# Kernel tuning notes

Hardware: AMD Instinct MI355X
Metric: run time of the kernel (lower is better)

The kernel has to match this reference:

```python
import jax, jax.numpy as jnp
import numpy as np

B, G, D = 256, 64, 20          # batch, genes per term, subsystem output dim
T3, T2, T1, T0 = 2048, 512, 128, 1  # terms per stratum, deepest first
FAN = 4                        # children per internal term (root gets all T1)
EPS = 1e-5                     # BatchNorm1d eps


def setup_inputs() -> dict:
    key = jax.random.key(0)
    ks = jax.random.split(key, 32)
    def genes(k, T):
        # binary gene perturbation states (column 3 of go_gene_strata_state)
        return (jax.random.uniform(k, (B, T, G)) < 0.5).astype(jnp.float32)
    def lin(kw, kb, T, din):
        # nn.init.uniform_(w, -0.001, 0.001) per DCellSubsystem
        W = jax.random.uniform(kw, (T, din, D), minval=-0.001, maxval=0.001)
        b = jax.random.uniform(kb, (T, D), minval=-0.001, maxval=0.001)
        return W, b
    in3, in2, in1, in0 = G, FAN * D + G, FAN * D + G, T1 * D + G
    W3, b3 = lin(ks[0], ks[1], T3, in3)
    W2, b2 = lin(ks[2], ks[3], T2, in2)
    W1, b1 = lin(ks[4], ks[5], T1, in1)
    W0, b0 = lin(ks[6], ks[7], T0, in0)
    ones = lambda T: jnp.ones((T, D), jnp.float32)
    zeros = lambda T: jnp.zeros((T, D), jnp.float32)
    hw0 = jax.random.normal(ks[8], (T0, D, 1)) * 0.1
    hb0 = jnp.zeros((T0, 1), jnp.float32)
    return {
        'genes3': genes(ks[9], T3), 'genes2': genes(ks[10], T2),
        'genes1': genes(ks[11], T1), 'genes0': genes(ks[12], T0),
        'W3': W3, 'b3': b3, 'g3': ones(T3), 'be3': zeros(T3),
        'W2': W2, 'b2': b2, 'g2': ones(T2), 'be2': zeros(T2),
        'W1': W1, 'b1': b1, 'g1': ones(T1), 'be1': zeros(T1),
        'W0': W0, 'b0': b0, 'g0': ones(T0), 'be0': zeros(T0),
        'hw0': hw0, 'hb0': hb0,
    }


def _subsystem(x, W, b, g, be):
    # Linear -> BatchNorm1d (training mode, batch stats over axis 0) -> Tanh
    z = jnp.einsum('bti,tio->bto', x, W) + b          # [B, T, D]
    mu = jnp.mean(z, axis=0)
    var = jnp.var(z, axis=0)                           # biased, as in torch BN
    zn = (z - mu) * jax.lax.rsqrt(var + EPS)
    return jnp.tanh(zn * g + be)


def reference(genes3, genes2, genes1, genes0,
              W3, b3, g3, be3, W2, b2, g2, be2,
              W1, b1, g1, be1, W0, b0, g0, be0, hw0, hb0):
    # stratum 3 (leaves): input is gene states only
    h3 = _subsystem(genes3, W3, b3, g3, be3)           # [B, T3, D]
    # stratum 2: concat FAN contiguous children + own gene states
    x2 = jnp.concatenate([h3.reshape(B, T2, FAN * D), genes2], axis=-1)
    h2 = _subsystem(x2, W2, b2, g2, be2)               # [B, T2, D]
    x1 = jnp.concatenate([h2.reshape(B, T1, FAN * D), genes1], axis=-1)
    h1 = _subsystem(x1, W1, b1, g1, be1)               # [B, T1, D]
    # root: all T1 children + root gene states
    x0 = jnp.concatenate([h1.reshape(B, T0, T1 * D), genes0], axis=-1)
    h0 = _subsystem(x0, W0, b0, g0, be0)               # [B, 1, D]
    pred = jnp.einsum('bto,toc->btc', h0, hw0) + hb0   # root linear head
    return pred.reshape(B, 1)
```

## Files before the change

### kernel.cpp

```cpp
#include <hip/hip_runtime.h>
#include <hip/hip_fp16.h>


#define DEV static __device__ __forceinline__

constexpr int B_  = 256, G_ = 64, D_ = 20;
constexpr int T3_ = 2048, T2_ = 512, T1_ = 128;
constexpr float EPS_ = 1e-5f;

typedef unsigned char u8;

constexpr size_t OFF_GT3 = 0;
constexpr size_t SZ_GT3 = (size_t)T3_ * B_ * G_;
constexpr size_t OFF_GT2 = OFF_GT3 + SZ_GT3;
constexpr size_t SZ_GT2 = (size_t)T2_ * B_ * G_;
constexpr size_t OFF_GT1 = OFF_GT2 + SZ_GT2;
constexpr size_t SZ_GT1 = (size_t)T1_ * B_ * G_;
constexpr size_t OFF_H3B = OFF_GT1 + SZ_GT1;
constexpr size_t SZ_H3 = (size_t)T3_ * B_ * D_ * 2;
constexpr size_t OFF_H2B = OFF_H3B + SZ_H3;
constexpr size_t SZ_H2 = (size_t)T2_ * B_ * D_ * 2;
constexpr size_t OFF_H1B = OFF_H2B + SZ_H2;
constexpr size_t SZ_H1 = (size_t)B_ * T1_ * D_ * 4;
constexpr size_t OFF_Z0B = OFF_H1B + SZ_H1;

typedef _Float16 half8_t __attribute__((ext_vector_type(8)));
typedef float f32x4 __attribute__((ext_vector_type(4)));

DEV half8_t as_h8(uint4 u) {
    union { uint4 u4; half8_t h; } c; c.u4 = u; return c.h;
}

DEV half8_t u8x8_to_h8(uint2 v) {
    uint4 r;
    uint x = v.x;
    r.x = ((x & 0xFFu) | ((x & 0xFF00u) << 8)) * 0x3C00u;
    r.y = (((x >> 16) & 0xFFu) | ((x >> 8) & 0xFF0000u)) * 0x3C00u;
    x = v.y;
    r.z = ((x & 0xFFu) | ((x & 0xFF00u) << 8)) * 0x3C00u;
    r.w = (((x >> 16) & 0xFFu) | ((x >> 8) & 0xFF0000u)) * 0x3C00u;
    return as_h8(r);
}

DEV float fast_tanh(float x) {
    float e = __expf(2.0f * x);
    return fmaf(-2.0f, __builtin_amdgcn_rcpf(e + 1.0f), 1.0f);
}

constexpr int TRB = 8;
constexpr int TRT = 64;
constexpr int LROW = TRT * G_ / 4 + 4;

__global__ __launch_bounds__(256, 4) void k_transpose_all(
        const float* __restrict__ g3s, const float* __restrict__ g2s,
        const float* __restrict__ g1s,
        u8* __restrict__ d3, u8* __restrict__ d2, u8* __restrict__ d1) {
    __shared__ uint lds[TRB * LROW];
    int blk = blockIdx.x;
    const float* src; u8* dst; int T;
    constexpr int NB3 = (T3_ / TRT) * (B_ / TRB);
    constexpr int NB2 = (T2_ / TRT) * (B_ / TRB);
    if (blk < NB3)              { src = g3s; dst = d3; T = T3_; }
    else if (blk < NB3 + NB2)   { blk -= NB3; src = g2s; dst = d2; T = T2_; }
    else                        { blk -= NB3 + NB2; src = g1s; dst = d1; T = T1_; }
    const int b0 = (blk & 31) * TRB;
    const int t0 = (blk >> 5) * TRT;
    const int tid = threadIdx.x;

#pragma unroll
    for (int it = 0; it < 32; ++it) {
        const int j = it * 256 + tid;
        const int r = j >> 10, off = j & 1023;
        float4 f = ((const float4*)(src + ((size_t)(b0 + r) * T + t0) * G_))[off];
        uint p = (uint)(u8)f.x | ((uint)(u8)f.y << 8) |
                 ((uint)(u8)f.z << 16) | ((uint)(u8)f.w << 24);
        lds[r * LROW + off] = p;
    }
    __syncthreads();

#pragma unroll
    for (int it = 0; it < 8; ++it) {
        const int j = it * 256 + tid;
        const int t = j >> 5, r = (j >> 2) & 7, c = j & 3;
        const uint* row = lds + r * LROW + t * 16 + c * 4;
        uint4 v = make_uint4(row[0], row[1], row[2], row[3]);
        ((uint4*)(dst + (((size_t)(t0 + t) * B_) + b0 + r) * G_))[c] = v;
    }
}

template <int T, int NCHILD, bool OUT_HALF>
__global__ __launch_bounds__(256, 4) void k_gemm(const __half* __restrict__ hsrc,
                                                 const u8* __restrict__ gT,
                                                 const float* __restrict__ W,
                                                 const float* __restrict__ g,
                                                 const float* __restrict__ be,
                                                 void* __restrict__ hout_) {
    constexpr int K_IN = NCHILD * 20 + 64;
    constexpr int NK = NCHILD + 2;
    constexpr int STRB = NCHILD ? 200 : 72;
    __shared__ __half WT[32 * STRB];
    __shared__ float gv[D_], bev[D_];
    __shared__ float sred[4][16], qred[4][16];

    const int t = blockIdx.x, tid = threadIdx.x;

    uint* WTu = (uint*)WT;
    for (int j = tid; j < 32 * STRB / 2; j += 256) WTu[j] = 0;
    if (tid < D_) { gv[tid] = g[t * D_ + tid]; bev[tid] = be[t * D_ + tid]; }
    __syncthreads();
    const float* Wt = W + (size_t)t * (K_IN * D_);
    for (int j = tid; j < K_IN * D_; j += 256) {
        int k_orig = j / D_, o = j - k_orig * D_;
        int k_lds;
        if (NCHILD && k_orig < NCHILD * D_) {
            int c = k_orig / D_;
            k_lds = c * 32 + (k_orig - c * D_);
        } else {
            k_lds = NCHILD * 32 + (k_orig - NCHILD * D_);
        }
        WT[o * STRB + k_lds] = __float2half(Wt[j]);
    }
    __syncthreads();

    const int w = tid >> 6, lane = tid & 63;
    const int quad = lane >> 4, l15 = lane & 15;
    const int nt = w >> 1, mhalf = w & 1;
    const int ocol = nt * 16 + l15;
    const int brow_base = mhalf * 128;

    half8_t Bf[NK];
#pragma unroll
    for (int ks = 0; ks < NK; ++ks)
        Bf[ks] = as_h8(*(const uint4*)(WT + ocol * STRB + ks * 32 + quad * 8));

    f32x4 acc[8];
#pragma unroll
    for (int mt = 0; mt < 8; ++mt) acc[mt] = (f32x4){0.f, 0.f, 0.f, 0.f};

#pragma unroll
    for (int mt = 0; mt < 8; ++mt) {
        const int bA = brow_base + mt * 16 + l15;
#pragma unroll
        for (int c = 0; c < NCHILD; ++c) {
            const __half* ap = hsrc + ((size_t)(NCHILD * t + c) * B_ + bA) * D_ + quad * 8;
            uint2 u0 = *(const uint2*)(ap);
            uint2 u1 = *(const uint2*)(ap + 4);
            acc[mt] = __builtin_amdgcn_mfma_f32_16x16x32_f16(
                as_h8(make_uint4(u0.x, u0.y, u1.x, u1.y)), Bf[c], acc[mt], 0, 0, 0);
        }
        const u8* gp = gT + ((size_t)t * B_ + bA) * G_ + quad * 8;
#pragma unroll
        for (int ks = 0; ks < 2; ++ks) {
            uint2 au = *(const uint2*)(gp + ks * 32);
            acc[mt] = __builtin_amdgcn_mfma_f32_16x16x32_f16(
                u8x8_to_h8(au), Bf[NCHILD + ks], acc[mt], 0, 0, 0);
        }
    }

    float s = 0.f, q = 0.f;
#pragma unroll
    for (int mt = 0; mt < 8; ++mt)
#pragma unroll
        for (int r = 0; r < 4; ++r) {
            float z = acc[mt][r];
            s += z; q += z * z;
        }
    s += __shfl_xor(s, 16, 64); q += __shfl_xor(q, 16, 64);
    s += __shfl_xor(s, 32, 64); q += __shfl_xor(q, 32, 64);
    if (lane < 16) { sred[w][lane] = s; qred[w][lane] = q; }
    __syncthreads();
    const float S = sred[2 * nt][l15] + sred[2 * nt + 1][l15];
    const float Q = qred[2 * nt][l15] + qred[2 * nt + 1][l15];
    const float mu  = S * (1.0f / B_);
    const float var = fmaxf(Q * (1.0f / B_) - mu * mu, 0.0f);
    const float rstd = rsqrtf(var + EPS_);
    const int oc = ocol < D_ ? ocol : D_ - 1;
    const float A = rstd * gv[oc];
    const float C = bev[oc] - mu * A;

    if (ocol < D_) {
#pragma unroll
        for (int mt = 0; mt < 8; ++mt)
#pragma unroll
            for (int r = 0; r < 4; ++r) {
                float h = fast_tanh(fmaf(A, acc[mt][r], C));
                int b = brow_base + mt * 16 + quad * 4 + r;
                if (OUT_HALF) {
                    ((__half*)hout_)[((size_t)t * B_ + b) * D_ + ocol] = __float2half(h);
                } else {
                    ((float*)hout_)[((size_t)b * T + t) * D_ + ocol] = h;
                }
            }
    }
}

__global__ __launch_bounds__(256, 4) void k_stage0a(const float* __restrict__ h1,
                                                    const float* __restrict__ genes0,
                                                    const float* __restrict__ W0,
                                                    float* __restrict__ z0p) {
    const int b = blockIdx.x >> 2, s = blockIdx.x & 3, tid = threadIdx.x;
    const int kbase = 640 * s;
    const float* x = h1 + (size_t)b * (T1_ * D_);
    float acc[D_] = {};
#pragma unroll
    for (int j = 0; j < 3; ++j) {
        int kl = tid + 256 * j;
        if (kl < 640) {
            int k = kbase + kl;
            float xk = x[k];
            const float4* w = (const float4*)(W0 + (size_t)k * D_);
#pragma unroll
            for (int v = 0; v < D_ / 4; ++v) {
                float4 f = w[v];
                acc[4 * v + 0] = fmaf(xk, f.x, acc[4 * v + 0]);
                acc[4 * v + 1] = fmaf(xk, f.y, acc[4 * v + 1]);
                acc[4 * v + 2] = fmaf(xk, f.z, acc[4 * v + 2]);
                acc[4 * v + 3] = fmaf(xk, f.w, acc[4 * v + 3]);
            }
        }
    }
    if (s == 3 && tid < G_) {
        float xk = genes0[(size_t)b * G_ + tid];
        const float4* w = (const float4*)(W0 + (size_t)(T1_ * D_ + tid) * D_);
#pragma unroll
        for (int v = 0; v < D_ / 4; ++v) {
            float4 f = w[v];
            acc[4 * v + 0] = fmaf(xk, f.x, acc[4 * v + 0]);
            acc[4 * v + 1] = fmaf(xk, f.y, acc[4 * v + 1]);
            acc[4 * v + 2] = fmaf(xk, f.z, acc[4 * v + 2]);
            acc[4 * v + 3] = fmaf(xk, f.w, acc[4 * v + 3]);
        }
    }
    __shared__ float sred[4][D_];
    const int lane = tid & 63, wave = tid >> 6;
#pragma unroll
    for (int off = 32; off; off >>= 1)
#pragma unroll
        for (int o = 0; o < D_; ++o) acc[o] += __shfl_xor(acc[o], off, 64);
    if (lane == 0)
#pragma unroll
        for (int o = 0; o < D_; ++o) sred[wave][o] = acc[o];
    __syncthreads();
    if (tid < D_)
        z0p[((size_t)b * 4 + s) * D_ + tid] =
            sred[0][tid] + sred[1][tid] + sred[2][tid] + sred[3][tid];
}

__global__ __launch_bounds__(256) void k_stage0b(const float* __restrict__ z0p,
                                                 const float* __restrict__ g0,
                                                 const float* __restrict__ be0,
                                                 const float* __restrict__ hw0,
                                                 const float* __restrict__ hb0,
                                                 float* __restrict__ out) {
    const int tid = threadIdx.x;
    float acc[D_] = {};
#pragma unroll
    for (int s = 0; s < 4; ++s) {
        const float4* zp = (const float4*)(z0p + ((size_t)tid * 4 + s) * D_);
#pragma unroll
        for (int v = 0; v < D_ / 4; ++v) {
            float4 f = zp[v];
            acc[4 * v + 0] += f.x; acc[4 * v + 1] += f.y;
            acc[4 * v + 2] += f.z; acc[4 * v + 3] += f.w;
        }
    }
    __shared__ float sred[4][D_], qred[4][D_], Avec[D_], Cvec[D_], hwv[D_ + 1];
    const int lane = tid & 63, wave = tid >> 6;
    float s[D_], q[D_];
#pragma unroll
    for (int o = 0; o < D_; ++o) { s[o] = acc[o]; q[o] = acc[o] * acc[o]; }
#pragma unroll
    for (int off = 32; off; off >>= 1) {
#pragma unroll
        for (int o = 0; o < D_; ++o) {
            s[o] += __shfl_xor(s[o], off, 64);
            q[o] += __shfl_xor(q[o], off, 64);
        }
    }
    if (lane == 0) {
#pragma unroll
        for (int o = 0; o < D_; ++o) { sred[wave][o] = s[o]; qred[wave][o] = q[o]; }
    }
    __syncthreads();
    if (tid < D_) {
        float S = sred[0][tid] + sred[1][tid] + sred[2][tid] + sred[3][tid];
        float Q = qred[0][tid] + qred[1][tid] + qred[2][tid] + qred[3][tid];
        float mu  = S * (1.0f / B_);
        float var = fmaxf(Q * (1.0f / B_) - mu * mu, 0.0f);
        float rstd = rsqrtf(var + EPS_);
        float A = rstd * g0[tid];
        Avec[tid] = A;
        Cvec[tid] = be0[tid] - mu * A;
        hwv[tid] = hw0[tid];
    }
    if (tid == 0) hwv[D_] = hb0[0];
    __syncthreads();
    float pred = hwv[D_];
#pragma unroll
    for (int o = 0; o < D_; ++o) {
        float h = fast_tanh(fmaf(acc[o], Avec[o], Cvec[o]));
        pred = fmaf(h, hwv[o], pred);
    }
    out[tid] = pred;
}

extern "C" void kernel_launch(void* const* d_in, const int* in_sizes, int n_in,
                              void* d_out, int out_size, void* d_ws, size_t ws_size,
                              hipStream_t stream) {
    const float* genes3 = (const float*)d_in[0];
    const float* genes2 = (const float*)d_in[1];
    const float* genes1 = (const float*)d_in[2];
    const float* genes0 = (const float*)d_in[3];
    const float* W3  = (const float*)d_in[4];
    const float* g3  = (const float*)d_in[6];
    const float* be3 = (const float*)d_in[7];
    const float* W2  = (const float*)d_in[8];
    const float* g2  = (const float*)d_in[10];
    const float* be2 = (const float*)d_in[11];
    const float* W1  = (const float*)d_in[12];
    const float* g1  = (const float*)d_in[14];
    const float* be1 = (const float*)d_in[15];
    const float* W0  = (const float*)d_in[16];
    const float* g0  = (const float*)d_in[18];
    const float* be0 = (const float*)d_in[19];
    const float* hw0 = (const float*)d_in[20];
    const float* hb0 = (const float*)d_in[21];

    char* wsb = (char*)d_ws;
    u8* gT3 = (u8*)(wsb + OFF_GT3);
    u8* gT2 = (u8*)(wsb + OFF_GT2);
    u8* gT1 = (u8*)(wsb + OFF_GT1);
    __half* h3  = (__half*)(wsb + OFF_H3B);
    __half* h2  = (__half*)(wsb + OFF_H2B);
    float*  h1  = (float*)(wsb + OFF_H1B);
    float*  z0p = (float*)(wsb + OFF_Z0B);

    constexpr int NTB = (T3_ / TRT + T2_ / TRT + T1_ / TRT) * (B_ / TRB);
    k_transpose_all<<<NTB, 256, 0, stream>>>(genes3, genes2, genes1, gT3, gT2, gT1);
    k_gemm<T3_, 0, true ><<<T3_, 256, 0, stream>>>(nullptr, gT3, W3, g3, be3, h3);
    k_gemm<T2_, 4, true ><<<T2_, 256, 0, stream>>>(h3, gT2, W2, g2, be2, h2);
    k_gemm<T1_, 4, false><<<T1_, 256, 0, stream>>>(h2, gT1, W1, g1, be1, h1);
    k_stage0a<<<B_ * 4, 256, 0, stream>>>(h1, genes0, W0, z0p);
    k_stage0b<<<1, 256, 0, stream>>>(z0p, g0, be0, hw0, hb0, (float*)d_out);
}
```

Measured before the change: 347.7 us.

## Pack binary gene states into 64-bit masks instead of byte transposes

The transpose kernel now turns each (batch, term) row of 64 float gene states into one 64-bit bitmask, stored term-major, instead of a 64-byte u8 copy. The GEMM kernels load one uint2 per row and expand 8 bits at a time into fp16 MFMA operands, with new bit-to-half conversion logic. This cuts the workspace write and re-read traffic for gene states about eightfold and drops the large LDS staging tile. The cost is that it relies on gene inputs being strictly binary (it tests for nonzero) and adds a little ALU work to unpack bits.

```diff
diff --git a/kernel.cpp b/kernel.cpp
--- a/kernel.cpp
+++ b/kernel.cpp
@@ -9,14 +9,15 @@
 constexpr float EPS_ = 1e-5f;
 
 typedef unsigned char u8;
-
-constexpr size_t OFF_GT3 = 0;
-constexpr size_t SZ_GT3 = (size_t)T3_ * B_ * G_;
-constexpr size_t OFF_GT2 = OFF_GT3 + SZ_GT3;
-constexpr size_t SZ_GT2 = (size_t)T2_ * B_ * G_;
-constexpr size_t OFF_GT1 = OFF_GT2 + SZ_GT2;
-constexpr size_t SZ_GT1 = (size_t)T1_ * B_ * G_;
-constexpr size_t OFF_H3B = OFF_GT1 + SZ_GT1;
+typedef unsigned long long u64;
+
+constexpr size_t OFF_GTB3 = 0;
+constexpr size_t SZ_GTB3 = (size_t)T3_ * B_ * 8;
+constexpr size_t OFF_GTB2 = OFF_GTB3 + SZ_GTB3;
+constexpr size_t SZ_GTB2 = (size_t)T2_ * B_ * 8;
+constexpr size_t OFF_GTB1 = OFF_GTB2 + SZ_GTB2;
+constexpr size_t SZ_GTB1 = (size_t)T1_ * B_ * 8;
+constexpr size_t OFF_H3B = OFF_GTB1 + SZ_GTB1;
 constexpr size_t SZ_H3 = (size_t)T3_ * B_ * D_ * 2;
 constexpr size_t OFF_H2B = OFF_H3B + SZ_H3;
 constexpr size_t SZ_H2 = (size_t)T2_ * B_ * D_ * 2;
@@ -31,14 +32,12 @@
     union { uint4 u4; half8_t h; } c; c.u4 = u; return c.h;
 }
 
-DEV half8_t u8x8_to_h8(uint2 v) {
+DEV half8_t bits8_to_h8(uint byte) {
     uint4 r;
-    uint x = v.x;
-    r.x = ((x & 0xFFu) | ((x & 0xFF00u) << 8)) * 0x3C00u;
-    r.y = (((x >> 16) & 0xFFu) | ((x >> 8) & 0xFF0000u)) * 0x3C00u;
-    x = v.y;
-    r.z = ((x & 0xFFu) | ((x & 0xFF00u) << 8)) * 0x3C00u;
-    r.w = (((x >> 16) & 0xFFu) | ((x >> 8) & 0xFF0000u)) * 0x3C00u;
+    r.x = ((byte & 1u)        | ((byte & 2u)   << 15)) * 0x3C00u;
+    r.y = (((byte >> 2) & 1u) | ((byte & 8u)   << 13)) * 0x3C00u;
+    r.z = (((byte >> 4) & 1u) | ((byte & 32u)  << 11)) * 0x3C00u;
+    r.w = (((byte >> 6) & 1u) | ((byte & 128u) << 9))  * 0x3C00u;
     return as_h8(r);
 }
 
@@ -47,50 +46,40 @@
     return fmaf(-2.0f, __builtin_amdgcn_rcpf(e + 1.0f), 1.0f);
 }
 
-constexpr int TRB = 8;
-constexpr int TRT = 64;
-constexpr int LROW = TRT * G_ / 4 + 4;
-
-__global__ __launch_bounds__(256, 4) void k_transpose_all(
+__global__ __launch_bounds__(256, 8) void k_transpose_all(
         const float* __restrict__ g3s, const float* __restrict__ g2s,
         const float* __restrict__ g1s,
-        u8* __restrict__ d3, u8* __restrict__ d2, u8* __restrict__ d1) {
-    __shared__ uint lds[TRB * LROW];
+        u64* __restrict__ d3, u64* __restrict__ d2, u64* __restrict__ d1) {
+    __shared__ uint nib[2048 + 128];
     int blk = blockIdx.x;
-    const float* src; u8* dst; int T;
-    constexpr int NB3 = (T3_ / TRT) * (B_ / TRB);
-    constexpr int NB2 = (T2_ / TRT) * (B_ / TRB);
-    if (blk < NB3)              { src = g3s; dst = d3; T = T3_; }
-    else if (blk < NB3 + NB2)   { blk -= NB3; src = g2s; dst = d2; T = T2_; }
-    else                        { blk -= NB3 + NB2; src = g1s; dst = d1; T = T1_; }
-    const int b0 = (blk & 31) * TRB;
-    const int t0 = (blk >> 5) * TRT;
+    const float* src; u64* dst; int T, b, tc;
+    if (blk < 4096)      { src = g3s; dst = d3; T = T3_; b = blk >> 4; tc = blk & 15; }
+    else if (blk < 5120) { blk -= 4096; src = g2s; dst = d2; T = T2_; b = blk >> 2; tc = blk & 3; }
+    else                 { blk -= 5120; src = g1s; dst = d1; T = T1_; b = blk; tc = 0; }
     const int tid = threadIdx.x;
-
-#pragma unroll
-    for (int it = 0; it < 32; ++it) {
-        const int j = it * 256 + tid;
-        const int r = j >> 10, off = j & 1023;
-        float4 f = ((const float4*)(src + ((size_t)(b0 + r) * T + t0) * G_))[off];
-        uint p = (uint)(u8)f.x | ((uint)(u8)f.y << 8) |
-                 ((uint)(u8)f.z << 16) | ((uint)(u8)f.w << 24);
-        lds[r * LROW + off] = p;
-    }
-    __syncthreads();
-
+    const float4* base = (const float4*)(src + ((size_t)b * T + tc * 128) * G_);
 #pragma unroll
     for (int it = 0; it < 8; ++it) {
         const int j = it * 256 + tid;
-        const int t = j >> 5, r = (j >> 2) & 7, c = j & 3;
-        const uint* row = lds + r * LROW + t * 16 + c * 4;
-        uint4 v = make_uint4(row[0], row[1], row[2], row[3]);
-        ((uint4*)(dst + (((size_t)(t0 + t) * B_) + b0 + r) * G_))[c] = v;
+        float4 f = base[j];
+        uint m = (f.x != 0.f ? 1u : 0u) | (f.y != 0.f ? 2u : 0u) |
+                 (f.z != 0.f ? 4u : 0u) | (f.w != 0.f ? 8u : 0u);
+        nib[j + (j >> 4)] = m;
+    }
+    __syncthreads();
+    if (tid < 128) {
+        const uint* p = nib + 17 * tid;
+        uint lo = p[0]        | (p[1] << 4)  | (p[2] << 8)   | (p[3] << 12) |
+                  (p[4] << 16) | (p[5] << 20) | (p[6] << 24) | (p[7] << 28);
+        uint hi = p[8]        | (p[9] << 4)  | (p[10] << 8)  | (p[11] << 12) |
+                  (p[12] << 16)| (p[13] << 20)| (p[14] << 24)| (p[15] << 28);
+        dst[(size_t)(tc * 128 + tid) * B_ + b] = (u64)lo | ((u64)hi << 32);
     }
 }
 
 template <int T, int NCHILD, bool OUT_HALF>
 __global__ __launch_bounds__(256, 4) void k_gemm(const __half* __restrict__ hsrc,
-                                                 const u8* __restrict__ gT,
+                                                 const u64* __restrict__ gTb,
                                                  const float* __restrict__ W,
                                                  const float* __restrict__ g,
                                                  const float* __restrict__ be,
@@ -127,6 +116,7 @@
     const int nt = w >> 1, mhalf = w & 1;
     const int ocol = nt * 16 + l15;
     const int brow_base = mhalf * 128;
+    const int shq = quad * 8;
 
     half8_t Bf[NK];
 #pragma unroll
@@ -140,6 +130,7 @@
 #pragma unroll
     for (int mt = 0; mt < 8; ++mt) {
         const int bA = brow_base + mt * 16 + l15;
+        const uint2 gu = ((const uint2*)gTb)[(size_t)t * B_ + bA];
 #pragma unroll
         for (int c = 0; c < NCHILD; ++c) {
             const __half* ap = hsrc + ((size_t)(NCHILD * t + c) * B_ + bA) * D_ + quad * 8;
@@ -148,13 +139,10 @@
             acc[mt] = __builtin_amdgcn_mfma_f32_16x16x32_f16(
                 as_h8(make_uint4(u0.x, u0.y, u1.x, u1.y)), Bf[c], acc[mt], 0, 0, 0);
         }
-        const u8* gp = gT + ((size_t)t * B_ + bA) * G_ + quad * 8;
-#pragma unroll
-        for (int ks = 0; ks < 2; ++ks) {
-            uint2 au = *(const uint2*)(gp + ks * 32);
-            acc[mt] = __builtin_amdgcn_mfma_f32_16x16x32_f16(
-                u8x8_to_h8(au), Bf[NCHILD + ks], acc[mt], 0, 0, 0);
-        }
+        acc[mt] = __builtin_amdgcn_mfma_f32_16x16x32_f16(
+            bits8_to_h8((gu.x >> shq) & 0xFFu), Bf[NCHILD], acc[mt], 0, 0, 0);
+        acc[mt] = __builtin_amdgcn_mfma_f32_16x16x32_f16(
+            bits8_to_h8((gu.y >> shq) & 0xFFu), Bf[NCHILD + 1], acc[mt], 0, 0, 0);
     }
 
     float s = 0.f, q = 0.f;
@@ -327,19 +315,19 @@
     const float* hb0 = (const float*)d_in[21];
 
     char* wsb = (char*)d_ws;
-    u8* gT3 = (u8*)(wsb + OFF_GT3);
-    u8* gT2 = (u8*)(wsb + OFF_GT2);
-    u8* gT1 = (u8*)(wsb + OFF_GT1);
+    u64* gTb3 = (u64*)(wsb + OFF_GTB3);
+    u64* gTb2 = (u64*)(wsb + OFF_GTB2);
+    u64* gTb1 = (u64*)(wsb + OFF_GTB1);
     __half* h3  = (__half*)(wsb + OFF_H3B);
     __half* h2  = (__half*)(wsb + OFF_H2B);
     float*  h1  = (float*)(wsb + OFF_H1B);
     float*  z0p = (float*)(wsb + OFF_Z0B);
 
-    constexpr int NTB = (T3_ / TRT + T2_ / TRT + T1_ / TRT) * (B_ / TRB);
-    k_transpose_all<<<NTB, 256, 0, stream>>>(genes3, genes2, genes1, gT3, gT2, gT1);
-    k_gemm<T3_, 0, true ><<<T3_, 256, 0, stream>>>(nullptr, gT3, W3, g3, be3, h3);
-    k_gemm<T2_, 4, true ><<<T2_, 256, 0, stream>>>(h3, gT2, W2, g2, be2, h2);
-    k_gemm<T1_, 4, false><<<T1_, 256, 0, stream>>>(h2, gT1, W1, g1, be1, h1);
+    k_transpose_all<<<4096 + 1024 + 256, 256, 0, stream>>>(genes3, genes2, genes1,
+                                                           gTb3, gTb2, gTb1);
+    k_gemm<T3_, 0, true ><<<T3_, 256, 0, stream>>>(nullptr, gTb3, W3, g3, be3, h3);
+    k_gemm<T2_, 4, true ><<<T2_, 256, 0, stream>>>(h3, gTb2, W2, g2, be2, h2);
+    k_gemm<T1_, 4, false><<<T1_, 256, 0, stream>>>(h2, gTb1, W1, g1, be1, h1);
     k_stage0a<<<B_ * 4, 256, 0, stream>>>(h1, genes0, W0, z0p);
     k_stage0b<<<1, 256, 0, stream>>>(z0p, g0, be0, hw0, hb0, (float*)d_out);
 }
```

Measured after the change: 324.7 us. -6.6%, faster.
